# Performance work log

Measured on AMD Instinct MI355X. Metric: run time of the kernel, lower is better.

The kernel has to match this reference:

```python
import jax, jax.numpy as jnp
import numpy as np

HEAD_DIM = 32
KERNEL = 3
DILATION = 2


def _unfold(x, k, dil):
    """torch.nn.Unfold with stride=1, padding=dil*(k-1)//2.
    x: [B, C, H, W] -> patches [B, C, k*k, H, W] (kernel positions row-major,
    channel-major overall, matching torch's (B, C*k*k, L) layout)."""
    B, C, H, W = x.shape
    pad = dil * (k - 1) // 2
    xp = jnp.pad(x, ((0, 0), (0, 0), (pad, pad), (pad, pad)))
    patches = jnp.stack(
        [xp[:, :, i * dil:i * dil + H, j * dil:j * dil + W]
         for i in range(k) for j in range(k)],
        axis=2,
    )
    return patches  # [B, C, k*k, H, W]


def setup_inputs() -> dict:
    key = jax.random.key(0)
    kq, kk, kv = jax.random.split(key, 3)
    shape = (8, 384, 56, 56)
    return {
        "q": jax.random.normal(kq, shape, dtype=jnp.float32),
        "k": jax.random.normal(kk, shape, dtype=jnp.float32),
        "v": jax.random.normal(kv, shape, dtype=jnp.float32),
    }


def reference(q, k, v):
    B, d, H, W = q.shape
    h = d // HEAD_DIM
    N = H * W
    k2 = KERNEL * KERNEL
    scale = HEAD_DIM ** (-0.5)

    # q: [B, h, N, hd]
    qr = q.reshape(B, h, HEAD_DIM, N).transpose(0, 1, 3, 2)
    # k patches: [B, h, hd, k2, N]
    kp = _unfold(k, KERNEL, DILATION).reshape(B, h, HEAD_DIM, k2, N)
    attn = jnp.einsum('bhnd,bhdkn->bhnk', qr, kp) * scale
    attn = jax.nn.softmax(attn, axis=-1)
    # v patches: [B, h, hd, k2, N]
    vp = _unfold(v, KERNEL, DILATION).reshape(B, h, HEAD_DIM, k2, N)
    out = jnp.einsum('bhnk,bhdkn->bhnd', attn, vp)  # [B, h, N, hd]
    # transpose(1,2) then reshape(B, H, W, d)
    return out.transpose(0, 2, 1, 3).reshape(B, H, W, d)
```

## Files before the change

kernel.cpp:

```cpp
#include <hip/hip_runtime.h>

#define HD 32
#define NHEADS 12
#define HH 56
#define WW 56
#define NN (HH * WW)
#define BB 8
#define CC (HD * NHEADS)
#define SCALE 0.17677669529663689f

__device__ __forceinline__ float dpp_up1(float x) {
    return __int_as_float(
        __builtin_amdgcn_update_dpp(0, __float_as_int(x), 0x138, 0xF, 0xF, true));
}
__device__ __forceinline__ float dpp_dn1(float x) {
    return __int_as_float(
        __builtin_amdgcn_update_dpp(0, __float_as_int(x), 0x130, 0xF, 0xF, true));
}

__global__ __launch_bounds__(256) void dilate_attn_kernel(
    const float* __restrict__ q,
    const float* __restrict__ k,
    const float* __restrict__ v,
    float* __restrict__ out)
{
    const int tx = threadIdx.x;
    const int qc = threadIdx.y;
    const int bh = blockIdx.y;
    const int b = bh / NHEADS;
    const int head = bh - b * NHEADS;

    const int n0r = blockIdx.x * 112 + 2 * tx;
    const int n0 = (n0r <= NN - 2) ? n0r : NN - 2;
    const bool active = (tx < 56);

    const int y  = n0 / WW;
    const int x0 = n0 - y * WW;
    const float mlo = (x0 == 0)      ? 0.f : 1.f;
    const float mhi = (x0 == WW - 2) ? 0.f : 1.f;

    const int base0 = (b * CC + head * HD + qc * 8) * NN;

    __shared__ float2 part[4][64][9];

    float2 qv[8];
#pragma unroll
    for (int d = 0; d < 8; ++d)
        qv[d] = *reinterpret_cast<const float2*>(q + base0 + d * NN + n0);

    float rm[3]; int rb[3];
#pragma unroll
    for (int r = 0; r < 3; ++r) {
        const int ny = y + (r - 1) * 2;
        rm[r] = ((unsigned)ny < HH) ? 1.f : 0.f;
        const int nyc = ny < 0 ? 0 : (ny > HH - 1 ? HH - 1 : ny);
        rb[r] = base0 + nyc * WW + x0;
    }

    float2 km[3][8];
#pragma unroll
    for (int r = 0; r < 3; ++r)
#pragma unroll
        for (int d = 0; d < 8; ++d)
            km[r][d] = *reinterpret_cast<const float2*>(k + rb[r] + d * NN);

    float2 vm[3][8];
#pragma unroll
    for (int r = 0; r < 3; ++r)
#pragma unroll
        for (int d = 0; d < 8; ++d)
            vm[r][d] = *reinterpret_cast<const float2*>(v + rb[r] + d * NN);

    float lg[9][2];
#pragma unroll
    for (int r = 0; r < 3; ++r) {
        float s0x = 0.f, s0y = 0.f, s1x = 0.f, s1y = 0.f, s2x = 0.f, s2y = 0.f;
#pragma unroll
        for (int d = 0; d < 8; ++d) {
            const float2 w1 = km[r][d];
            const float w0x = dpp_up1(w1.x);
            const float w0y = dpp_up1(w1.y);
            const float w2x = dpp_dn1(w1.x);
            const float w2y = dpp_dn1(w1.y);
            s0x = fmaf(qv[d].x, w0x, s0x);  s0y = fmaf(qv[d].y, w0y, s0y);
            s1x = fmaf(qv[d].x, w1.x, s1x); s1y = fmaf(qv[d].y, w1.y, s1y);
            s2x = fmaf(qv[d].x, w2x, s2x);  s2y = fmaf(qv[d].y, w2y, s2y);
        }
        const float m0 = rm[r] * mlo, m2 = rm[r] * mhi;
        lg[r * 3 + 0][0] = s0x * m0;    lg[r * 3 + 0][1] = s0y * m0;
        lg[r * 3 + 1][0] = s1x * rm[r]; lg[r * 3 + 1][1] = s1y * rm[r];
        lg[r * 3 + 2][0] = s2x * m2;    lg[r * 3 + 2][1] = s2y * m2;
    }

#pragma unroll
    for (int t = 0; t < 9; ++t) part[qc][tx][t] = make_float2(lg[t][0], lg[t][1]);
    __syncthreads();
#pragma unroll
    for (int o = 1; o < 4; ++o) {
        const int oq = (qc + o) & 3;
#pragma unroll
        for (int t = 0; t < 9; ++t) {
            const float2 p = part[oq][tx][t];
            lg[t][0] += p.x; lg[t][1] += p.y;
        }
    }

#pragma unroll
    for (int j = 0; j < 2; ++j) {
        float m = lg[0][j] * SCALE;
#pragma unroll
        for (int t = 0; t < 9; ++t) { lg[t][j] *= SCALE; m = fmaxf(m, lg[t][j]); }
        float s = 0.f;
#pragma unroll
        for (int t = 0; t < 9; ++t) { const float e = __expf(lg[t][j] - m); lg[t][j] = e; s += e; }
        const float inv = 1.f / s;
#pragma unroll
        for (int t = 0; t < 9; ++t) lg[t][j] *= inv;
    }
#pragma unroll
    for (int r = 0; r < 3; ++r) {
        const float m0 = rm[r] * mlo, m2 = rm[r] * mhi;
        lg[r * 3 + 0][0] *= m0;    lg[r * 3 + 0][1] *= m0;
        lg[r * 3 + 1][0] *= rm[r]; lg[r * 3 + 1][1] *= rm[r];
        lg[r * 3 + 2][0] *= m2;    lg[r * 3 + 2][1] *= m2;
    }

    float acc[8][2];
#pragma unroll
    for (int d = 0; d < 8; ++d) { acc[d][0] = 0.f; acc[d][1] = 0.f; }
#pragma unroll
    for (int r = 0; r < 3; ++r) {
        const float g0x = lg[r * 3 + 0][0], g0y = lg[r * 3 + 0][1];
        const float g1x = lg[r * 3 + 1][0], g1y = lg[r * 3 + 1][1];
        const float g2x = lg[r * 3 + 2][0], g2y = lg[r * 3 + 2][1];
#pragma unroll
        for (int d = 0; d < 8; ++d) {
            const float2 u1 = vm[r][d];
            const float u0x = dpp_up1(u1.x);
            const float u0y = dpp_up1(u1.y);
            const float u2x = dpp_dn1(u1.x);
            const float u2y = dpp_dn1(u1.y);
            acc[d][0] = fmaf(g0x, u0x, acc[d][0]);  acc[d][1] = fmaf(g0y, u0y, acc[d][1]);
            acc[d][0] = fmaf(g1x, u1.x, acc[d][0]); acc[d][1] = fmaf(g1y, u1.y, acc[d][1]);
            acc[d][0] = fmaf(g2x, u2x, acc[d][0]);  acc[d][1] = fmaf(g2y, u2y, acc[d][1]);
        }
    }

    if (active) {
#pragma unroll
        for (int j = 0; j < 2; ++j) {
            float* ob = out + ((b * HH + y) * WW + (x0 + j)) * CC + head * HD + qc * 8;
            *reinterpret_cast<float4*>(ob)     = make_float4(acc[0][j], acc[1][j], acc[2][j], acc[3][j]);
            *reinterpret_cast<float4*>(ob + 4) = make_float4(acc[4][j], acc[5][j], acc[6][j], acc[7][j]);
        }
    }
}

extern "C" void kernel_launch(void* const* d_in, const int* in_sizes, int n_in,
                              void* d_out, int out_size, void* d_ws, size_t ws_size,
                              hipStream_t stream) {
    const float* q = (const float*)d_in[0];
    const float* k = (const float*)d_in[1];
    const float* v = (const float*)d_in[2];
    float* out = (float*)d_out;

    dim3 block(64, 4);
    dim3 grid(NN / 112, BB * NHEADS);
    dilate_attn_kernel<<<grid, block, 0, stream>>>(q, k, v, out);
}
```

Before: 167.4 us.

## Split head channels across 8 groups, defer V loads, remap blocks for XCD locality

Each block now has 8 channel groups of 4 channels instead of 4 groups of 8, which halves per-thread register use for q/k/v tiles and doubles threads per block. V loads are moved after the logit barrier so they overlap with the cross-group reduction, with a sched_barrier that keeps the compiler from hoisting them back. A flattened grid with an XCD-aware remap keeps neighbouring stripes of the same batch-head on one chiplet for cache locality. The cost is a larger cross-group LDS reduction (8-way instead of 4-way) and half-width output stores per thread.

```diff
diff --git a/kernel.cpp b/kernel.cpp
--- a/kernel.cpp
+++ b/kernel.cpp
@@ -8,6 +8,8 @@
 #define BB 8
 #define CC (HD * NHEADS)
 #define SCALE 0.17677669529663689f
+#define NGR 8
+#define GCH 4
 
 __device__ __forceinline__ float dpp_up1(float x) {
     return __int_as_float(
@@ -18,7 +20,7 @@
         __builtin_amdgcn_update_dpp(0, __float_as_int(x), 0x130, 0xF, 0xF, true));
 }
 
-__global__ __launch_bounds__(256) void dilate_attn_kernel(
+__global__ __launch_bounds__(512) void dilate_attn_kernel(
     const float* __restrict__ q,
     const float* __restrict__ k,
     const float* __restrict__ v,
@@ -26,11 +28,14 @@
 {
     const int tx = threadIdx.x;
     const int qc = threadIdx.y;
-    const int bh = blockIdx.y;
+    const int flat = blockIdx.x;
+    const int work = (flat & 7) * 336 + (flat >> 3);
+    const int stripe = work % 28;
+    const int bh     = work / 28;
     const int b = bh / NHEADS;
     const int head = bh - b * NHEADS;
 
-    const int n0r = blockIdx.x * 112 + 2 * tx;
+    const int n0r = stripe * 112 + 2 * tx;
     const int n0 = (n0r <= NN - 2) ? n0r : NN - 2;
     const bool active = (tx < 56);
 
@@ -39,13 +44,13 @@
     const float mlo = (x0 == 0)      ? 0.f : 1.f;
     const float mhi = (x0 == WW - 2) ? 0.f : 1.f;
 
-    const int base0 = (b * CC + head * HD + qc * 8) * NN;
+    const int base0 = (b * CC + head * HD + qc * GCH) * NN;
 
-    __shared__ float2 part[4][64][9];
+    __shared__ float2 part[NGR][64][9];
 
-    float2 qv[8];
+    float2 qv[GCH];
 #pragma unroll
-    for (int d = 0; d < 8; ++d)
+    for (int d = 0; d < GCH; ++d)
         qv[d] = *reinterpret_cast<const float2*>(q + base0 + d * NN + n0);
 
     float rm[3]; int rb[3];
@@ -57,26 +62,19 @@
         rb[r] = base0 + nyc * WW + x0;
     }
 
-    float2 km[3][8];
+    float2 km[3][GCH];
 #pragma unroll
     for (int r = 0; r < 3; ++r)
 #pragma unroll
-        for (int d = 0; d < 8; ++d)
+        for (int d = 0; d < GCH; ++d)
             km[r][d] = *reinterpret_cast<const float2*>(k + rb[r] + d * NN);
-
-    float2 vm[3][8];
-#pragma unroll
-    for (int r = 0; r < 3; ++r)
-#pragma unroll
-        for (int d = 0; d < 8; ++d)
-            vm[r][d] = *reinterpret_cast<const float2*>(v + rb[r] + d * NN);
 
     float lg[9][2];
 #pragma unroll
     for (int r = 0; r < 3; ++r) {
         float s0x = 0.f, s0y = 0.f, s1x = 0.f, s1y = 0.f, s2x = 0.f, s2y = 0.f;
 #pragma unroll
-        for (int d = 0; d < 8; ++d) {
+        for (int d = 0; d < GCH; ++d) {
             const float2 w1 = km[r][d];
             const float w0x = dpp_up1(w1.x);
             const float w0y = dpp_up1(w1.y);
@@ -95,9 +93,18 @@
 #pragma unroll
     for (int t = 0; t < 9; ++t) part[qc][tx][t] = make_float2(lg[t][0], lg[t][1]);
     __syncthreads();
+
+    float2 vm[3][GCH];
 #pragma unroll
-    for (int o = 1; o < 4; ++o) {
-        const int oq = (qc + o) & 3;
+    for (int r = 0; r < 3; ++r)
+#pragma unroll
+        for (int d = 0; d < GCH; ++d)
+            vm[r][d] = *reinterpret_cast<const float2*>(v + rb[r] + d * NN);
+    __builtin_amdgcn_sched_barrier(0);
+
+#pragma unroll
+    for (int o = 1; o < NGR; ++o) {
+        const int oq = (qc + o) & (NGR - 1);
 #pragma unroll
         for (int t = 0; t < 9; ++t) {
             const float2 p = part[oq][tx][t];
@@ -125,16 +132,16 @@
         lg[r * 3 + 2][0] *= m2;    lg[r * 3 + 2][1] *= m2;
     }
 
-    float acc[8][2];
+    float acc[GCH][2];
 #pragma unroll
-    for (int d = 0; d < 8; ++d) { acc[d][0] = 0.f; acc[d][1] = 0.f; }
+    for (int d = 0; d < GCH; ++d) { acc[d][0] = 0.f; acc[d][1] = 0.f; }
 #pragma unroll
     for (int r = 0; r < 3; ++r) {
         const float g0x = lg[r * 3 + 0][0], g0y = lg[r * 3 + 0][1];
         const float g1x = lg[r * 3 + 1][0], g1y = lg[r * 3 + 1][1];
         const float g2x = lg[r * 3 + 2][0], g2y = lg[r * 3 + 2][1];
 #pragma unroll
-        for (int d = 0; d < 8; ++d) {
+        for (int d = 0; d < GCH; ++d) {
             const float2 u1 = vm[r][d];
             const float u0x = dpp_up1(u1.x);
             const float u0y = dpp_up1(u1.y);
@@ -149,9 +156,9 @@
     if (active) {
 #pragma unroll
         for (int j = 0; j < 2; ++j) {
-            float* ob = out + ((b * HH + y) * WW + (x0 + j)) * CC + head * HD + qc * 8;
-            *reinterpret_cast<float4*>(ob)     = make_float4(acc[0][j], acc[1][j], acc[2][j], acc[3][j]);
-            *reinterpret_cast<float4*>(ob + 4) = make_float4(acc[4][j], acc[5][j], acc[6][j], acc[7][j]);
+            float* ob = out + ((b * HH + y) * WW + (x0 + j)) * CC + head * HD + qc * GCH;
+            *reinterpret_cast<float4*>(ob) =
+                make_float4(acc[0][j], acc[1][j], acc[2][j], acc[3][j]);
         }
     }
 }
@@ -164,7 +171,7 @@
     const float* v = (const float*)d_in[2];
     float* out = (float*)d_out;
 
-    dim3 block(64, 4);
-    dim3 grid(NN / 112, BB * NHEADS);
+    dim3 block(64, NGR);
+    dim3 grid(28 * BB * NHEADS);
     dilate_attn_kernel<<<grid, block, 0, stream>>>(q, k, v, out);
 }
```

Result: no change. 169.6 us (+1.3%).
